# Kernel tuning notes

Measured on AMD Instinct MI355X. Metric: run time of the kernel, lower is better.

Reference implementation:

```python
import jax, jax.numpy as jnp
import numpy as np
from jax import lax

K = 3
STRIDE = 2
PADDING = 1
OUTPUT_PADDING = 1


def setup_inputs() -> dict:
    key = jax.random.key(0)
    k1, k2, k3, k4 = jax.random.split(key, 4)
    B, C, H, W = 4, 64, 128, 128
    outC = 64
    g_ch = 3
    x = jax.random.normal(k1, (B, C, H, W), dtype=jnp.float32)
    guide = jax.random.normal(k2, (B, g_ch, H * STRIDE, W * STRIDE), dtype=jnp.float32)
    # kaiming-uniform-like init scale: bound = 1/sqrt(fan_in), fan_in = C*K*K
    fan_in = C * K * K
    bound = 1.0 / np.sqrt(fan_in)
    weight = jax.random.uniform(k3, (C, outC, K, K), dtype=jnp.float32, minval=-bound, maxval=bound)
    bias = jax.random.uniform(k4, (outC,), dtype=jnp.float32, minval=-bound, maxval=bound)
    return {"x": x, "guide": guide, "weight": weight, "bias": bias}


def _patches(t, pad):
    # torch.nn.functional.unfold equivalent: channel ordering (C, kh, kw)
    return lax.conv_general_dilated_patches(
        t, filter_shape=(K, K), window_strides=(1, 1), padding=[(pad, pad), (pad, pad)]
    )


def reference(x, guide, weight, bias):
    B, C, H, W = x.shape
    _, g_ch, GH, GW = guide.shape
    s, p, op = STRIDE, PADDING, OUTPUT_PADDING

    # Gaussian affinity kernel from guide patches
    gp = (K - 1) // 2
    guide_unf = _patches(guide, gp).reshape(B, g_ch, K * K, GH, GW)
    diff = guide_unf - guide_unf[:, :, K * K // 2 : K * K // 2 + 1]
    kern = jnp.exp(-0.5 * jnp.sum(diff * diff, axis=1))  # [B, K*K, GH, GW]
    kern = kern.reshape(B, 1, K, K, GH, GW)

    # depthwise transposed conv with all-ones 1x1 kernel == zero-stuffing upsample
    Ht, Wt = (H - 1) * s + 1, (W - 1) * s + 1
    temp = jnp.zeros((B, C, Ht, Wt), dtype=x.dtype).at[:, :, ::s, ::s].set(x)
    pad = (K - 1) - p
    temp = jnp.pad(temp, ((0, 0), (0, 0), (pad, pad + op), (pad, pad + op)))

    cols = _patches(temp, 0).reshape(B, C, K, K, GH, GW)
    in_mul_k = cols * kern  # [B, C, K, K, GH, GW]
    out = jnp.einsum("bcklhw,cokl->bohw", in_mul_k, weight)
    return out + bias.reshape(1, -1, 1, 1)
```

## Files before the change

### kernel.cpp

```cpp
#include <hip/hip_runtime.h>
#include <math.h>

typedef __attribute__((ext_vector_type(8))) short short8;
typedef __attribute__((ext_vector_type(4))) float float4v;

#define GH_ 256
#define GW_ 256
#define H_  128
#define W_  128
#define C_  64
#define OC_ 64
#define NB_ 4

static __device__ __forceinline__ unsigned short f2bf(float f) {
    union { float f; unsigned int u; } v; v.f = f;
    unsigned int u = v.u;
    unsigned int r = u + 0x7FFFu + ((u >> 16) & 1u);
    return (unsigned short)(r >> 16);
}

__global__ __launch_bounds__(256) void prep(const float* __restrict__ x,
                                            const float* __restrict__ w,
                                            unsigned short* __restrict__ xbf,
                                            unsigned short* __restrict__ wtb) {
    int b = blockIdx.z;
    int tid = threadIdx.x;
    if (b == 4) {
        int flat = (blockIdx.y * 2 + blockIdx.x) * 256 + tid;
        if (flat < 9 * OC_ * C_) {
            int c = flat & 63, o = (flat >> 6) & 63, t = flat >> 12;
            int kh = t / 3, kw = t - kh * 3;
            wtb[flat] = f2bf(w[((c * OC_ + o) * 3 + kh) * 3 + kw]);
        }
        return;
    }
    int half = blockIdx.x, ih = blockIdx.y;
    __shared__ float xl[C_][65];
    int iw0 = half * 64;
    for (int i = tid; i < C_ * 64; i += 256) {
        int c = i >> 6, iw = i & 63;
        xl[c][iw] = x[(((b * C_ + c) * H_) + ih) * W_ + iw0 + iw];
    }
    __syncthreads();
    for (int i = tid; i < 64 * 32; i += 256) {
        int iw = i >> 5, cp = i & 31;
        unsigned int lo = f2bf(xl[2 * cp][iw]);
        unsigned int hi = f2bf(xl[2 * cp + 1][iw]);
        unsigned int* dst = (unsigned int*)(xbf +
            ((size_t)((b * H_ + ih) * W_ + iw0 + iw)) * C_);
        dst[cp] = lo | (hi << 16);
    }
}

__global__ __launch_bounds__(512, 2) void pac_main(
    const unsigned short* __restrict__ xbf,
    const float* __restrict__ guide,
    const unsigned short* __restrict__ wtb,
    const float* __restrict__ bias,
    float* __restrict__ out)
{
    const int ypair = blockIdx.x;
    const int hp    = blockIdx.y;
    const int b     = blockIdx.z;
    const int tid = threadIdx.x;
    const int ntr = 1 + hp;
    const int nslot = 3 * ntr;

    __shared__ float klds[6][2][128];

    for (int i = tid; i < nslot * 256; i += 512) {
        int px = i & 255, slot = i >> 8;
        int py = px >> 7, xp = px & 127;
        int wp, r, q;
        if (slot < ntr) { wp = 0; r = slot; q = 0; }
        else { int s = slot - ntr; wp = 1; r = s >> 1; q = s & 1; }
        int yp = ypair * 2 + py;
        int h = 2 * yp + hp, w = 2 * xp + wp;
        int rr = yp + r, cl = xp + q;
        float kv = 0.f;
        if (rr < H_ && cl < W_) {
            int hh = rr * 2, ww = cl * 2;
            const float* gb = guide + (size_t)b * 3 * GH_ * GW_;
            float s2 = 0.f;
            #pragma unroll
            for (int g = 0; g < 3; ++g) {
                float d = gb[(g * GH_ + hh) * GW_ + ww] - gb[(g * GH_ + h) * GW_ + w];
                s2 += d * d;
            }
            kv = __expf(-0.5f * s2);
        }
        klds[slot][py][xp] = kv;
    }
    __syncthreads();

    const int wave = tid >> 6, lane = tid & 63;
    const int l16 = lane & 15, qk = lane >> 4;
    const int oh  = wave & 1;
    const int py  = (wave >> 1) & 1;
    const int xh  = wave >> 2;
    const int obase = oh * 32;
    const int xpb   = xh * 64;
    const int yp = ypair * 2 + py;
    const int h  = 2 * yp + hp;

    float acc0[2][4][4];
    float acc1[2][4][4];
    #pragma unroll
    for (int mf = 0; mf < 2; ++mf)
        #pragma unroll
        for (int nf = 0; nf < 4; ++nf)
            #pragma unroll
            for (int e = 0; e < 4; ++e) { acc0[mf][nf][e] = 0.f; acc1[mf][nf][e] = 0.f; }

    for (int r = 0; r <= hp; ++r) {
        int kh = hp ? 2 * r : 1;
        int row = yp + r; if (row > H_ - 1) row = H_ - 1;
        int s_c = r;
        int s_l = ntr + 2 * r;
        int s_r = ntr + 2 * r + 1;

        short8 af[3][2][2];
        #pragma unroll
        for (int kw3 = 0; kw3 < 3; ++kw3) {
            const short8* wbase = (const short8*)(wtb + (size_t)(kh * 3 + kw3) * OC_ * C_);
            #pragma unroll
            for (int mf = 0; mf < 2; ++mf) {
                int o = obase + mf * 16 + l16;
                af[kw3][mf][0] = wbase[(o * C_ + qk * 8) >> 3];
                af[kw3][mf][1] = wbase[(o * C_ + 32 + qk * 8) >> 3];
            }
        }

        #pragma unroll
        for (int nf = 0; nf < 4; ++nf) {
            int xp = xpb + nf * 16 + l16;
            int col0 = xp;
            int col1 = xp + 1; if (col1 > W_ - 1) col1 = W_ - 1;
            const short8* xb0 = (const short8*)(xbf +
                ((size_t)((b * H_ + row) * W_ + col0)) * C_);
            const short8* xb1 = (const short8*)(xbf +
                ((size_t)((b * H_ + row) * W_ + col1)) * C_);
            short8 b0a = xb0[qk],     b0b = xb0[4 + qk];
            short8 b1a = xb1[qk],     b1b = xb1[4 + qk];
            float kc = klds[s_c][py][xp];
            float kl = klds[s_l][py][xp];
            float kr = klds[s_r][py][xp];
            #pragma unroll
            for (int mf = 0; mf < 2; ++mf) {
                float4v d;
                d = (float4v){0.f, 0.f, 0.f, 0.f};
                d = __builtin_amdgcn_mfma_f32_16x16x32_bf16(af[1][mf][0], b0a, d, 0, 0, 0);
                d = __builtin_amdgcn_mfma_f32_16x16x32_bf16(af[1][mf][1], b0b, d, 0, 0, 0);
                #pragma unroll
                for (int e = 0; e < 4; ++e) acc0[mf][nf][e] += kc * d[e];
                d = (float4v){0.f, 0.f, 0.f, 0.f};
                d = __builtin_amdgcn_mfma_f32_16x16x32_bf16(af[0][mf][0], b0a, d, 0, 0, 0);
                d = __builtin_amdgcn_mfma_f32_16x16x32_bf16(af[0][mf][1], b0b, d, 0, 0, 0);
                #pragma unroll
                for (int e = 0; e < 4; ++e) acc1[mf][nf][e] += kl * d[e];
                d = (float4v){0.f, 0.f, 0.f, 0.f};
                d = __builtin_amdgcn_mfma_f32_16x16x32_bf16(af[2][mf][0], b1a, d, 0, 0, 0);
                d = __builtin_amdgcn_mfma_f32_16x16x32_bf16(af[2][mf][1], b1b, d, 0, 0, 0);
                #pragma unroll
                for (int e = 0; e < 4; ++e) acc1[mf][nf][e] += kr * d[e];
            }
        }
    }

    float bv[2][4];
    #pragma unroll
    for (int mf = 0; mf < 2; ++mf)
        #pragma unroll
        for (int e = 0; e < 4; ++e)
            bv[mf][e] = bias[obase + mf * 16 + qk * 4 + e];

    #pragma unroll
    for (int mf = 0; mf < 2; ++mf)
        #pragma unroll
        for (int e = 0; e < 4; ++e) {
            int o = obase + mf * 16 + qk * 4 + e;
            float2* op = (float2*)(out + (((size_t)b * OC_ + o) * GH_ + h) * GW_);
            #pragma unroll
            for (int nf = 0; nf < 4; ++nf) {
                int xp = xpb + nf * 16 + l16;
                float2 v;
                v.x = acc0[mf][nf][e] + bv[mf][e];
                v.y = acc1[mf][nf][e] + bv[mf][e];
                op[xp] = v;
            }
        }
}

extern "C" void kernel_launch(void* const* d_in, const int* in_sizes, int n_in,
                              void* d_out, int out_size, void* d_ws, size_t ws_size,
                              hipStream_t stream) {
    const float* x     = (const float*)d_in[0];
    const float* guide = (const float*)d_in[1];
    const float* wgt   = (const float*)d_in[2];
    const float* bias  = (const float*)d_in[3];
    float* out = (float*)d_out;

    unsigned short* xbf = (unsigned short*)d_ws;
    unsigned short* wtb = xbf + (size_t)NB_ * H_ * W_ * C_;

    prep<<<dim3(2, 128, 5), 256, 0, stream>>>(x, wgt, xbf, wtb);
    pac_main<<<dim3(64, 2, 4), 512, 0, stream>>>(xbf, guide, wtb, bias, out);
}
```

Before: 121.4 us.

## Split output-channel fragments into outer loop to raise occupancy; vectorize prep loads

The main kernel now handles its two 16-channel output fragments one after another in an outer loop, which halves the live accumulator and weight-fragment registers, and the launch bound asks for 4 blocks per CU instead of 2. In exchange, the activation tiles and affinity values are reloaded once per fragment, roughly doubling those loads. Grid dimensions are swapped so batch and parity map to different block axes. The prep kernel reads x with float4 loads instead of scalar loads.

```diff
diff --git a/kernel.cpp b/kernel.cpp
--- a/kernel.cpp
+++ b/kernel.cpp
@@ -37,9 +37,15 @@
     int half = blockIdx.x, ih = blockIdx.y;
     __shared__ float xl[C_][65];
     int iw0 = half * 64;
-    for (int i = tid; i < C_ * 64; i += 256) {
-        int c = i >> 6, iw = i & 63;
-        xl[c][iw] = x[(((b * C_ + c) * H_) + ih) * W_ + iw0 + iw];
+    for (int i = tid; i < C_ * 16; i += 256) {
+        int c = i >> 4, f4 = i & 15;
+        const float4* src = (const float4*)(x +
+            (((size_t)(b * C_ + c) * H_) + ih) * W_ + iw0 + f4 * 4);
+        float4 rd = *src;
+        xl[c][f4 * 4 + 0] = rd.x;
+        xl[c][f4 * 4 + 1] = rd.y;
+        xl[c][f4 * 4 + 2] = rd.z;
+        xl[c][f4 * 4 + 3] = rd.w;
     }
     __syncthreads();
     for (int i = tid; i < 64 * 32; i += 256) {
@@ -52,7 +58,7 @@
     }
 }
 
-__global__ __launch_bounds__(512, 2) void pac_main(
+__global__ __launch_bounds__(512, 4) void pac_main(
     const unsigned short* __restrict__ xbf,
     const float* __restrict__ guide,
     const unsigned short* __restrict__ wtb,
@@ -60,8 +66,8 @@
     float* __restrict__ out)
 {
     const int ypair = blockIdx.x;
-    const int hp    = blockIdx.y;
-    const int b     = blockIdx.z;
+    const int b     = blockIdx.y;
+    const int hp    = blockIdx.z;
     const int tid = threadIdx.x;
     const int ntr = 1 + hp;
     const int nslot = 3 * ntr;
@@ -103,92 +109,83 @@
     const int yp = ypair * 2 + py;
     const int h  = 2 * yp + hp;
 
-    float acc0[2][4][4];
-    float acc1[2][4][4];
-    #pragma unroll
-    for (int mf = 0; mf < 2; ++mf)
+    for (int mf = 0; mf < 2; ++mf) {
+        float acc0[4][4];
+        float acc1[4][4];
         #pragma unroll
         for (int nf = 0; nf < 4; ++nf)
             #pragma unroll
-            for (int e = 0; e < 4; ++e) { acc0[mf][nf][e] = 0.f; acc1[mf][nf][e] = 0.f; }
-
-    for (int r = 0; r <= hp; ++r) {
-        int kh = hp ? 2 * r : 1;
-        int row = yp + r; if (row > H_ - 1) row = H_ - 1;
-        int s_c = r;
-        int s_l = ntr + 2 * r;
-        int s_r = ntr + 2 * r + 1;
-
-        short8 af[3][2][2];
-        #pragma unroll
-        for (int kw3 = 0; kw3 < 3; ++kw3) {
-            const short8* wbase = (const short8*)(wtb + (size_t)(kh * 3 + kw3) * OC_ * C_);
-            #pragma unroll
-            for (int mf = 0; mf < 2; ++mf) {
-                int o = obase + mf * 16 + l16;
-                af[kw3][mf][0] = wbase[(o * C_ + qk * 8) >> 3];
-                af[kw3][mf][1] = wbase[(o * C_ + 32 + qk * 8) >> 3];
-            }
-        }
-
-        #pragma unroll
-        for (int nf = 0; nf < 4; ++nf) {
-            int xp = xpb + nf * 16 + l16;
-            int col0 = xp;
-            int col1 = xp + 1; if (col1 > W_ - 1) col1 = W_ - 1;
-            const short8* xb0 = (const short8*)(xbf +
-                ((size_t)((b * H_ + row) * W_ + col0)) * C_);
-            const short8* xb1 = (const short8*)(xbf +
-                ((size_t)((b * H_ + row) * W_ + col1)) * C_);
-            short8 b0a = xb0[qk],     b0b = xb0[4 + qk];
-            short8 b1a = xb1[qk],     b1b = xb1[4 + qk];
-            float kc = klds[s_c][py][xp];
-            float kl = klds[s_l][py][xp];
-            float kr = klds[s_r][py][xp];
-            #pragma unroll
-            for (int mf = 0; mf < 2; ++mf) {
+            for (int e = 0; e < 4; ++e) { acc0[nf][e] = 0.f; acc1[nf][e] = 0.f; }
+
+        const int o = obase + mf * 16 + l16;
+
+        for (int r = 0; r <= hp; ++r) {
+            int kh = hp ? 2 * r : 1;
+            int row = yp + r; if (row > H_ - 1) row = H_ - 1;
+            int s_c = r;
+            int s_l = ntr + 2 * r;
+            int s_r = ntr + 2 * r + 1;
+
+            short8 af[3][2];
+            #pragma unroll
+            for (int kw3 = 0; kw3 < 3; ++kw3) {
+                const short8* wbase = (const short8*)(wtb + (size_t)(kh * 3 + kw3) * OC_ * C_);
+                af[kw3][0] = wbase[(o * C_ + qk * 8) >> 3];
+                af[kw3][1] = wbase[(o * C_ + 32 + qk * 8) >> 3];
+            }
+
+            #pragma unroll
+            for (int nf = 0; nf < 4; ++nf) {
+                int xp = xpb + nf * 16 + l16;
+                int col0 = xp;
+                int col1 = xp + 1; if (col1 > W_ - 1) col1 = W_ - 1;
+                const short8* xb0 = (const short8*)(xbf +
+                    ((size_t)((b * H_ + row) * W_ + col0)) * C_);
+                const short8* xb1 = (const short8*)(xbf +
+                    ((size_t)((b * H_ + row) * W_ + col1)) * C_);
+                short8 b0a = xb0[qk],     b0b = xb0[4 + qk];
+                short8 b1a = xb1[qk],     b1b = xb1[4 + qk];
+                float kc = klds[s_c][py][xp];
+                float kl = klds[s_l][py][xp];
+                float kr = klds[s_r][py][xp];
                 float4v d;
                 d = (float4v){0.f, 0.f, 0.f, 0.f};
-                d = __builtin_amdgcn_mfma_f32_16x16x32_bf16(af[1][mf][0], b0a, d, 0, 0, 0);
-                d = __builtin_amdgcn_mfma_f32_16x16x32_bf16(af[1][mf][1], b0b, d, 0, 0, 0);
+                d = __builtin_amdgcn_mfma_f32_16x16x32_bf16(af[1][0], b0a, d, 0, 0, 0);
+                d = __builtin_amdgcn_mfma_f32_16x16x32_bf16(af[1][1], b0b, d, 0, 0, 0);
                 #pragma unroll
-                for (int e = 0; e < 4; ++e) acc0[mf][nf][e] += kc * d[e];
+                for (int e = 0; e < 4; ++e) acc0[nf][e] += kc * d[e];
                 d = (float4v){0.f, 0.f, 0.f, 0.f};
-                d = __builtin_amdgcn_mfma_f32_16x16x32_bf16(af[0][mf][0], b0a, d, 0, 0, 0);
-                d = __builtin_amdgcn_mfma_f32_16x16x32_bf16(af[0][mf][1], b0b, d, 0, 0, 0);
+                d = __builtin_amdgcn_mfma_f32_16x16x32_bf16(af[0][0], b0a, d, 0, 0, 0);
+                d = __builtin_amdgcn_mfma_f32_16x16x32_bf16(af[0][1], b0b, d, 0, 0, 0);
                 #pragma unroll
-                for (int e = 0; e < 4; ++e) acc1[mf][nf][e] += kl * d[e];
+                for (int e = 0; e < 4; ++e) acc1[nf][e] += kl * d[e];
                 d = (float4v){0.f, 0.f, 0.f, 0.f};
-                d = __builtin_amdgcn_mfma_f32_16x16x32_bf16(af[2][mf][0], b1a, d, 0, 0, 0);
-                d = __builtin_amdgcn_mfma_f32_16x16x32_bf16(af[2][mf][1], b1b, d, 0, 0, 0);
+                d = __builtin_amdgcn_mfma_f32_16x16x32_bf16(af[2][0], b1a, d, 0, 0, 0);
+                d = __builtin_amdgcn_mfma_f32_16x16x32_bf16(af[2][1], b1b, d, 0, 0, 0);
                 #pragma unroll
-                for (int e = 0; e < 4; ++e) acc1[mf][nf][e] += kr * d[e];
-            }
-        }
-    }
-
-    float bv[2][4];
-    #pragma unroll
-    for (int mf = 0; mf < 2; ++mf)
+                for (int e = 0; e < 4; ++e) acc1[nf][e] += kr * d[e];
+            }
+        }
+
+        float bv[4];
         #pragma unroll
         for (int e = 0; e < 4; ++e)
-            bv[mf][e] = bias[obase + mf * 16 + qk * 4 + e];
-
-    #pragma unroll
-    for (int mf = 0; mf < 2; ++mf)
+            bv[e] = bias[obase + mf * 16 + qk * 4 + e];
+
         #pragma unroll
         for (int e = 0; e < 4; ++e) {
-            int o = obase + mf * 16 + qk * 4 + e;
-            float2* op = (float2*)(out + (((size_t)b * OC_ + o) * GH_ + h) * GW_);
+            int oo = obase + mf * 16 + qk * 4 + e;
+            float2* op = (float2*)(out + (((size_t)b * OC_ + oo) * GH_ + h) * GW_);
             #pragma unroll
             for (int nf = 0; nf < 4; ++nf) {
                 int xp = xpb + nf * 16 + l16;
                 float2 v;
-                v.x = acc0[mf][nf][e] + bv[mf][e];
-                v.y = acc1[mf][nf][e] + bv[mf][e];
+                v.x = acc0[nf][e] + bv[e];
+                v.y = acc1[nf][e] + bv[e];
                 op[xp] = v;
             }
         }
+    }
 }
 
 extern "C" void kernel_launch(void* const* d_in, const int* in_sizes, int n_in,
@@ -204,5 +201,5 @@
     unsigned short* wtb = xbf + (size_t)NB_ * H_ * W_ * C_;
 
     prep<<<dim3(2, 128, 5), 256, 0, stream>>>(x, wgt, xbf, wtb);
-    pac_main<<<dim3(64, 2, 4), 512, 0, stream>>>(xbf, guide, wtb, bias, out);
-}
+    pac_main<<<dim3(64, 4, 2), 512, 0, stream>>>(xbf, guide, wtb, bias, out);
+}
```

After: 119.0 us. 1.02x faster.
